# Kernel optimization log

Hardware: AMD Instinct MI355X
Metric: run time of the kernel (lower is better)

Reference implementation:

```python
import jax, jax.numpy as jnp
import numpy as np

EMB = 256
HID = 256
NH = 8
HD = HID // NH  # 32
EPS = 1e-5


def _wn(v, g):
    # torch weight_norm(dim=0): per-output-row normalization of v
    return g[:, None] * v / jnp.linalg.norm(v, axis=1, keepdims=True)


def _ln(x, gamma, beta):
    mu = jnp.mean(x, axis=-1, keepdims=True)
    var = jnp.mean((x - mu) ** 2, axis=-1, keepdims=True)
    return (x - mu) * jax.lax.rsqrt(var + EPS) * gamma + beta


def _rope(x):
    # x: [B', S, H, D]; torchtune-style rotary embedding, base 10000
    S, D = x.shape[1], x.shape[3]
    freqs = 1.0 / (10000.0 ** (jnp.arange(0, D, 2, dtype=jnp.float32) / D))  # [D/2]
    ang = jnp.arange(S, dtype=jnp.float32)[:, None] * freqs[None, :]          # [S, D/2]
    cos = jnp.cos(ang)[None, :, None, :]
    sin = jnp.sin(ang)[None, :, None, :]
    xr = x.reshape(*x.shape[:-1], D // 2, 2)
    x0, x1 = xr[..., 0], xr[..., 1]
    out = jnp.stack([x0 * cos - x1 * sin, x1 * cos + x0 * sin], axis=-1)
    return out.reshape(x.shape)


def setup_inputs() -> dict:
    key = jax.random.key(0)
    ks = jax.random.split(key, 12)
    s = lambda shp: 0.02
    return {
        "z": jax.random.normal(ks[0], (2, 32, 512, EMB), dtype=jnp.float32),
        "ln1_g": jnp.ones((EMB,), jnp.float32),
        "ln1_b": jnp.zeros((EMB,), jnp.float32),
        "proj_v": jax.random.normal(ks[1], (3 * HID, EMB), jnp.float32) * 0.02,
        "proj_g": jnp.ones((3 * HID,), jnp.float32),
        "proj_b": jnp.zeros((3 * HID,), jnp.float32),
        "ff_v": jax.random.normal(ks[2], (EMB, HID), jnp.float32) * 0.02,
        "ff_g": jnp.ones((EMB,), jnp.float32),
        "ff_b": jnp.zeros((EMB,), jnp.float32),
        "ln2_g": jnp.ones((EMB,), jnp.float32),
        "ln2_b": jnp.zeros((EMB,), jnp.float32),
        "w1_v": jax.random.normal(ks[3], (EMB, EMB), jnp.float32) * 0.02,
        "w1_g": jnp.ones((EMB,), jnp.float32),
        "w1_b": jnp.zeros((EMB,), jnp.float32),
        "w2_v": jax.random.normal(ks[4], (EMB, EMB), jnp.float32) * 0.02,
        "w2_g": jnp.ones((EMB,), jnp.float32),
        "w2_b": jnp.zeros((EMB,), jnp.float32),
    }


def reference(z, ln1_g, ln1_b, proj_v, proj_g, proj_b, ff_v, ff_g, ff_b,
              ln2_g, ln2_b, w1_v, w1_g, w1_b, w2_v, w2_g, w2_b):
    B, U, A, E = z.shape
    BU = B * U
    Wqkv = _wn(proj_v, proj_g)   # [3H, E]
    Wo = _wn(ff_v, ff_g)         # [E, H]
    # ---- RoPE attention block ----
    z_ = _ln(z, ln1_g, ln1_b).reshape(BU, A, E)
    qkv = z_ @ Wqkv.T + proj_b                       # [BU, A, 3H]
    qkv = qkv.reshape(BU, A, NH, 3 * HD)
    q, k, v = jnp.split(qkv, 3, axis=-1)             # each [BU, A, NH, HD]
    q = _rope(q)
    k = _rope(k)
    qh = q.transpose(0, 2, 1, 3)                     # [BU, NH, A, HD]
    kh = k.transpose(0, 2, 1, 3)
    vh = v.transpose(0, 2, 1, 3)
    scores = jnp.einsum('bhqd,bhkd->bhqk', qh, kh) / jnp.sqrt(jnp.float32(HD))
    attn = jax.nn.softmax(scores, axis=-1)
    out = jnp.einsum('bhqk,bhkd->bhqd', attn, vh)    # [BU, NH, A, HD]
    out = out.transpose(0, 2, 1, 3).reshape(BU, A, HID)
    out = out @ Wo.T + ff_b
    z = z + out.reshape(B, U, A, E)
    # ---- NormFF block ----
    W1 = _wn(w1_v, w1_g)
    W2 = _wn(w2_v, w2_g)
    h = _ln(z, ln2_g, ln2_b)
    h = jax.nn.gelu(h @ W1.T + w1_b, approximate=False)
    h = h @ W2.T + w2_b
    return z + h
```

## Files before the change

kernel.cpp:

```cpp
#include <hip/hip_runtime.h>
#include <cmath>

#define EMB 256
#define NHEAD 8
#define HD 32
#define A_LEN 512
#define TOK 32768

typedef __bf16 bf16_t;
typedef __bf16 bf16x8 __attribute__((ext_vector_type(8)));
typedef __bf16 bf16x4 __attribute__((ext_vector_type(4)));
typedef float floatx4 __attribute__((ext_vector_type(4)));

#define MFMA16(a, b, c) __builtin_amdgcn_mfma_f32_16x16x32_bf16((a), (b), (c), 0, 0, 0)

__global__ __launch_bounds__(64) void setup_kernel(
    const float* __restrict__ proj_v, const float* __restrict__ proj_g,
    const float* __restrict__ ff_v, const float* __restrict__ ff_g,
    const float* __restrict__ w1_v, const float* __restrict__ w1_g,
    const float* __restrict__ w2_v, const float* __restrict__ w2_g,
    bf16_t* __restrict__ Wall, float* __restrict__ ctab,
    float* __restrict__ stab) {
    int b = blockIdx.x;
    int lane = threadIdx.x;
    if (b < 1536) {
        const float* v; const float* g; int r;
        if (b < 768)       { v = proj_v; g = proj_g; r = b; }
        else if (b < 1024) { v = ff_v;   g = ff_g;   r = b - 768; }
        else if (b < 1280) { v = w1_v;   g = w1_g;   r = b - 1024; }
        else               { v = w2_v;   g = w2_g;   r = b - 1280; }
        const floatx4* vr = (const floatx4*)(v + (size_t)r * 256);
        floatx4 x = vr[lane];
        float ss = x[0] * x[0] + x[1] * x[1] + x[2] * x[2] + x[3] * x[3];
#pragma unroll
        for (int off = 32; off >= 1; off >>= 1) ss += __shfl_xor(ss, off);
        float sc = g[r] * rsqrtf(ss);
        bf16x4 o;
        o[0] = (bf16_t)(x[0] * sc); o[1] = (bf16_t)(x[1] * sc);
        o[2] = (bf16_t)(x[2] * sc); o[3] = (bf16_t)(x[3] * sc);
        ((bf16x4*)(Wall + (size_t)b * 256))[lane] = o;
    } else {
        int idx = (b - 1536) * 64 + lane;
        int a = idx >> 4, i = idx & 15;
        float freq = expf(-(float)(2 * i) * 0.2878231366242558f);
        float ang = (float)a * freq;
        ctab[idx] = cosf(ang);
        stab[idx] = sinf(ang);
    }
}

__global__ __launch_bounds__(256, 4) void qkv_kernel(
    const float* __restrict__ z, const float* __restrict__ ln_g,
    const float* __restrict__ ln_b, const bf16_t* __restrict__ W,
    const float* __restrict__ pb, const float* __restrict__ ctab,
    const float* __restrict__ stab, bf16_t* __restrict__ qbf,
    bf16_t* __restrict__ kbf, bf16_t* __restrict__ vtb) {
    __shared__ bf16_t xns[32 * 264];
    __shared__ bf16_t vls[256 * 40];
    int tid = threadIdx.x;
    int t0 = blockIdx.x * 32;

#pragma unroll
    for (int it = 0; it < 2; ++it) {
        int row = it * 16 + (tid >> 4);
        int sub = tid & 15;
        const floatx4* zr = (const floatx4*)(z + (size_t)(t0 + row) * 256 + sub * 16);
        floatx4 v0 = zr[0], v1 = zr[1], v2 = zr[2], v3 = zr[3];
        float vals[16];
        ((floatx4*)vals)[0] = v0; ((floatx4*)vals)[1] = v1;
        ((floatx4*)vals)[2] = v2; ((floatx4*)vals)[3] = v3;
        float s = 0.f, q2 = 0.f;
#pragma unroll
        for (int i = 0; i < 16; ++i) { s += vals[i]; q2 += vals[i] * vals[i]; }
#pragma unroll
        for (int off = 8; off >= 1; off >>= 1) {
            s += __shfl_xor(s, off);
            q2 += __shfl_xor(q2, off);
        }
        float mu = s * (1.f / 256.f);
        float inv = rsqrtf(q2 * (1.f / 256.f) - mu * mu + 1e-5f);
        int cb = sub * 16;
        bf16x8 o0, o1;
#pragma unroll
        for (int i = 0; i < 8; ++i)
            o0[i] = (bf16_t)((vals[i] - mu) * inv * ln_g[cb + i] + ln_b[cb + i]);
#pragma unroll
        for (int i = 0; i < 8; ++i)
            o1[i] = (bf16_t)((vals[8 + i] - mu) * inv * ln_g[cb + 8 + i] + ln_b[cb + 8 + i]);
        *(bf16x8*)&xns[row * 264 + cb] = o0;
        *(bf16x8*)&xns[row * 264 + cb + 8] = o1;
    }
    __syncthreads();

    int wv = tid >> 6, lane = tid & 63, quad = lane >> 4, lidx = lane & 15;

#pragma unroll 1
    for (int g = 0; g < 3; ++g) {
        floatx4 acc[4][2];
#pragma unroll
        for (int i = 0; i < 4; ++i) {
            acc[i][0] = (floatx4){0.f, 0.f, 0.f, 0.f};
            acc[i][1] = (floatx4){0.f, 0.f, 0.f, 0.f};
        }
#pragma unroll 2
        for (int kc = 0; kc < 8; ++kc) {
            bf16x8 a0 = *(const bf16x8*)&xns[lidx * 264 + kc * 32 + quad * 8];
            bf16x8 a1 = *(const bf16x8*)&xns[(16 + lidx) * 264 + kc * 32 + quad * 8];
#pragma unroll
            for (int ntl = 0; ntl < 4; ++ntl) {
                int n = wv * 192 + (g * 4 + ntl) * 16 + lidx;
                bf16x8 bfr = *(const bf16x8*)&W[(size_t)n * 256 + kc * 32 + quad * 8];
                acc[ntl][0] = MFMA16(a0, bfr, acc[ntl][0]);
                acc[ntl][1] = MFMA16(a1, bfr, acc[ntl][1]);
            }
        }
#pragma unroll
        for (int ntl = 0; ntl < 4; ++ntl) {
            int nbase = wv * 192 + (g * 4 + ntl) * 16;
            int n = nbase + lidx;
            float bias = pb[n];
            int htile = nbase / 96;
            int rem = nbase % 96;
            int sec = rem >> 5;
            int d = (rem & 31) + lidx;
#pragma unroll
            for (int mt = 0; mt < 2; ++mt) {
#pragma unroll
                for (int r = 0; r < 4; ++r) {
                    int a_loc = mt * 16 + quad * 4 + r;
                    int tok = t0 + a_loc;
                    int a = tok & 511;
                    int bu = tok >> 9;
                    float val = acc[ntl][mt][r] + bias;
                    if (sec == 2) {
                        vls[(htile * 32 + d) * 40 + a_loc] = (bf16_t)val;
                    } else {
                        size_t addr = ((size_t)((bu * 8 + htile) * 512 + a)) * 32 + d;
                        float part = __shfl_xor(val, 1);
                        float cs = ctab[a * 16 + (d >> 1)];
                        float sn = stab[a * 16 + (d >> 1)];
                        float res = ((d & 1) == 0) ? (val * cs - part * sn)
                                                   : (val * cs + part * sn);
                        if (sec == 0)
                            qbf[addr] = (bf16_t)(res * 0.17677669529663687f);
                        else
                            kbf[addr] = (bf16_t)res;
                    }
                }
            }
        }
    }
    __syncthreads();
    {
        int bu = t0 >> 9, ac0 = t0 & 511;
        size_t gbase = ((size_t)(bu * 256 + tid)) * 512 + ac0;
#pragma unroll
        for (int j = 0; j < 4; ++j)
            *(bf16x8*)&vtb[gbase + j * 8] = *(const bf16x8*)&vls[tid * 40 + j * 8];
    }
}

__global__ __launch_bounds__(512, 4) void attn_kernel(
    const bf16_t* __restrict__ qbf, const bf16_t* __restrict__ kbf,
    const bf16_t* __restrict__ vtb, bf16_t* __restrict__ ob) {
    __shared__ bf16_t Kls[512 * 32];
    __shared__ bf16_t Vt[32 * 512];
    __shared__ bf16_t Pls[8 * 16 * 64];
    int tid = threadIdx.x;
    int wv = tid >> 6, lane = tid & 63, quad = lane >> 4, lidx = lane & 15;
    int bh = blockIdx.x;
    int bu = bh >> 3, h = bh & 7;
    size_t hb = (size_t)bh * (A_LEN * HD);

#pragma unroll
    for (int i = 0; i < 4; ++i) {
        int c = tid + i * 512;
        int key = c >> 2, blk = c & 3;
        bf16x8 kv = *(const bf16x8*)&kbf[hb + (size_t)c * 8];
        *(bf16x8*)&Kls[key * 32 + ((blk ^ (key & 3)) << 3)] = kv;
        int vrow = c >> 6, vblk = c & 63;
        bf16x8 vv = *(const bf16x8*)&vtb[hb + (size_t)c * 8];
        *(bf16x8*)&Vt[vrow * 512 + ((vblk ^ (vrow & 7)) << 3)] = vv;
    }
    __syncthreads();

    int pbase = wv * (16 * 64);
    const floatx4 cm8 = (floatx4){-8.f, -8.f, -8.f, -8.f};
    const floatx4 zero4 = (floatx4){0.f, 0.f, 0.f, 0.f};

#pragma unroll 1
    for (int mt = 0; mt < 4; ++mt) {
        int q0 = wv * 64 + mt * 16;
        bf16x8 qfrag = *(const bf16x8*)&qbf[hb + (size_t)(q0 + lidx) * 32 + quad * 8];
        float l_[4] = {0.f, 0.f, 0.f, 0.f};
        floatx4 Oacc[2];
        Oacc[0] = zero4; Oacc[1] = zero4;

#pragma unroll 1
        for (int kc = 0; kc < 8; ++kc) {
            floatx4 sc[4];
#pragma unroll
            for (int t = 0; t < 4; ++t) {
                bf16x8 kf = *(const bf16x8*)&Kls[(kc * 64 + t * 16 + lidx) * 32 +
                                                 ((quad ^ (lidx & 3)) << 3)];
                sc[t] = MFMA16(qfrag, kf, cm8);
            }
            float p[4][4];
#pragma unroll
            for (int t = 0; t < 4; ++t)
#pragma unroll
                for (int r = 0; r < 4; ++r) p[t][r] = __expf(sc[t][r]);
#pragma unroll
            for (int t = 0; t < 4; ++t)
#pragma unroll
                for (int r = 0; r < 4; ++r) {
                    int row = quad * 4 + r;
                    int pc = (t * 16 + lidx) ^ ((row & 7) << 3);
                    Pls[pbase + row * 64 + pc] = (bf16_t)p[t][r];
                }
#pragma unroll
            for (int r = 0; r < 4; ++r) {
                float s = (p[0][r] + p[1][r]) + (p[2][r] + p[3][r]);
#pragma unroll
                for (int off = 8; off >= 1; off >>= 1) s += __shfl_xor(s, off);
                l_[r] += s;
            }
#pragma unroll
            for (int ks = 0; ks < 2; ++ks) {
                bf16x8 pf = *(const bf16x8*)&Pls[pbase + lidx * 64 +
                                                 (((ks * 4 + quad) ^ (lidx & 7)) << 3)];
#pragma unroll
                for (int nt = 0; nt < 2; ++nt) {
                    int vrow = nt * 16 + lidx;
                    bf16x8 vf = *(const bf16x8*)&Vt[vrow * 512 +
                        ((kc * 8 + ((ks * 4 + quad) ^ (lidx & 7))) << 3)];
                    Oacc[nt] = MFMA16(pf, vf, Oacc[nt]);
                }
            }
        }
#pragma unroll
        for (int nt = 0; nt < 2; ++nt)
#pragma unroll
            for (int r = 0; r < 4; ++r) {
                int tok = bu * 512 + q0 + quad * 4 + r;
                ob[(size_t)tok * 256 + h * 32 + nt * 16 + lidx] =
                    (bf16_t)(Oacc[nt][r] / l_[r]);
            }
    }
}

__global__ __launch_bounds__(256, 4) void tail_kernel(
    const bf16_t* __restrict__ X, const bf16_t* __restrict__ Wo,
    const float* __restrict__ obias, const float* __restrict__ zin,
    const float* __restrict__ ln_g, const float* __restrict__ ln_b,
    const bf16_t* __restrict__ W1, const float* __restrict__ b1,
    const bf16_t* __restrict__ W2, const float* __restrict__ b2,
    float* __restrict__ outp) {
    __shared__ float fbuf[32 * 264];
    __shared__ float red[32 * 8];
    __shared__ float mi[32 * 2];
    bf16_t* xbuf = (bf16_t*)fbuf;
    int tid = threadIdx.x;
    int t0 = blockIdx.x * 32;
    int wv = tid >> 6, lane = tid & 63, quad = lane >> 4, lidx = lane & 15;

    {
        int row = tid >> 3;
        int c0 = (tid & 7) * 32;
        const bf16x8* src = (const bf16x8*)&X[(size_t)(t0 + row) * 256 + c0];
        bf16x8* dst = (bf16x8*)&xbuf[row * 264 + c0];
        dst[0] = src[0]; dst[1] = src[1]; dst[2] = src[2]; dst[3] = src[3];
    }
    __syncthreads();

    float r1[4][2][4];
    {
        floatx4 acc[4][2];
#pragma unroll
        for (int i = 0; i < 4; ++i) {
            acc[i][0] = (floatx4){0.f, 0.f, 0.f, 0.f};
            acc[i][1] = (floatx4){0.f, 0.f, 0.f, 0.f};
        }
#pragma unroll 2
        for (int kc = 0; kc < 8; ++kc) {
            bf16x8 a0 = *(const bf16x8*)&xbuf[lidx * 264 + kc * 32 + quad * 8];
            bf16x8 a1 = *(const bf16x8*)&xbuf[(16 + lidx) * 264 + kc * 32 + quad * 8];
#pragma unroll
            for (int nt = 0; nt < 4; ++nt) {
                int n = wv * 64 + nt * 16 + lidx;
                bf16x8 bfr = *(const bf16x8*)&Wo[(size_t)n * 256 + kc * 32 + quad * 8];
                acc[nt][0] = MFMA16(a0, bfr, acc[nt][0]);
                acc[nt][1] = MFMA16(a1, bfr, acc[nt][1]);
            }
        }
#pragma unroll
        for (int nt = 0; nt < 4; ++nt) {
            int n = wv * 64 + nt * 16 + lidx;
            float b = obias[n];
#pragma unroll
            for (int mt = 0; mt < 2; ++mt)
#pragma unroll
                for (int r = 0; r < 4; ++r) {
                    size_t o = (size_t)(t0 + mt * 16 + quad * 4 + r) * 256 + n;
                    r1[nt][mt][r] = zin[o] + acc[nt][mt][r] + b;
                }
        }
    }

#pragma unroll
    for (int mt = 0; mt < 2; ++mt)
#pragma unroll
        for (int r = 0; r < 4; ++r) {
            float s = 0.f, ss = 0.f;
#pragma unroll
            for (int nt = 0; nt < 4; ++nt) {
                float v = r1[nt][mt][r];
                s += v; ss += v * v;
            }
#pragma unroll
            for (int off = 8; off >= 1; off >>= 1) {
                s += __shfl_xor(s, off);
                ss += __shfl_xor(ss, off);
            }
            if (lidx == 0) {
                int row = mt * 16 + quad * 4 + r;
                red[row * 8 + wv * 2] = s;
                red[row * 8 + wv * 2 + 1] = ss;
            }
        }
    __syncthreads();
    if (tid < 32) {
        float s = 0.f, ss = 0.f;
#pragma unroll
        for (int w = 0; w < 4; ++w) {
            s += red[tid * 8 + w * 2];
            ss += red[tid * 8 + w * 2 + 1];
        }
        float mu = s * (1.f / 256.f);
        mi[tid * 2] = mu;
        mi[tid * 2 + 1] = rsqrtf(ss * (1.f / 256.f) - mu * mu + 1e-5f);
    }
    __syncthreads();

    {
        float gv[4], bv[4];
#pragma unroll
        for (int nt = 0; nt < 4; ++nt) {
            int n = wv * 64 + nt * 16 + lidx;
            gv[nt] = ln_g[n]; bv[nt] = ln_b[n];
        }
#pragma unroll
        for (int mt = 0; mt < 2; ++mt)
#pragma unroll
            for (int r = 0; r < 4; ++r) {
                int row = mt * 16 + quad * 4 + r;
                float mu = mi[row * 2], inv = mi[row * 2 + 1];
#pragma unroll
                for (int nt = 0; nt < 4; ++nt) {
                    int n = wv * 64 + nt * 16 + lidx;
                    xbuf[row * 264 + n] =
                        (bf16_t)((r1[nt][mt][r] - mu) * inv * gv[nt] + bv[nt]);
                }
            }
    }
    __syncthreads();

    {
        floatx4 acc[4][2];
#pragma unroll
        for (int i = 0; i < 4; ++i) {
            acc[i][0] = (floatx4){0.f, 0.f, 0.f, 0.f};
            acc[i][1] = (floatx4){0.f, 0.f, 0.f, 0.f};
        }
#pragma unroll 2
        for (int kc = 0; kc < 8; ++kc) {
            bf16x8 a0 = *(const bf16x8*)&xbuf[lidx * 264 + kc * 32 + quad * 8];
            bf16x8 a1 = *(const bf16x8*)&xbuf[(16 + lidx) * 264 + kc * 32 + quad * 8];
#pragma unroll
            for (int nt = 0; nt < 4; ++nt) {
                int n = wv * 64 + nt * 16 + lidx;
                bf16x8 bfr = *(const bf16x8*)&W1[(size_t)n * 256 + kc * 32 + quad * 8];
                acc[nt][0] = MFMA16(a0, bfr, acc[nt][0]);
                acc[nt][1] = MFMA16(a1, bfr, acc[nt][1]);
            }
        }
        __syncthreads();
#pragma unroll
        for (int nt = 0; nt < 4; ++nt) {
            int n = wv * 64 + nt * 16 + lidx;
            float b = b1[n];
#pragma unroll
            for (int mt = 0; mt < 2; ++mt)
#pragma unroll
                for (int r = 0; r < 4; ++r) {
                    float x = acc[nt][mt][r] + b;
                    float gel = 0.5f * x * (1.f + erff(x * 0.7071067811865476f));
                    xbuf[(mt * 16 + quad * 4 + r) * 264 + n] = (bf16_t)gel;
                }
        }
    }
    __syncthreads();

    {
        floatx4 acc[4][2];
#pragma unroll
        for (int i = 0; i < 4; ++i) {
            acc[i][0] = (floatx4){0.f, 0.f, 0.f, 0.f};
            acc[i][1] = (floatx4){0.f, 0.f, 0.f, 0.f};
        }
#pragma unroll 2
        for (int kc = 0; kc < 8; ++kc) {
            bf16x8 a0 = *(const bf16x8*)&xbuf[lidx * 264 + kc * 32 + quad * 8];
            bf16x8 a1 = *(const bf16x8*)&xbuf[(16 + lidx) * 264 + kc * 32 + quad * 8];
#pragma unroll
            for (int nt = 0; nt < 4; ++nt) {
                int n = wv * 64 + nt * 16 + lidx;
                bf16x8 bfr = *(const bf16x8*)&W2[(size_t)n * 256 + kc * 32 + quad * 8];
                acc[nt][0] = MFMA16(a0, bfr, acc[nt][0]);
                acc[nt][1] = MFMA16(a1, bfr, acc[nt][1]);
            }
        }
        __syncthreads();
#pragma unroll
        for (int nt = 0; nt < 4; ++nt) {
            int n = wv * 64 + nt * 16 + lidx;
            float b = b2[n];
#pragma unroll
            for (int mt = 0; mt < 2; ++mt)
#pragma unroll
                for (int r = 0; r < 4; ++r)
                    fbuf[(mt * 16 + quad * 4 + r) * 264 + n] =
                        r1[nt][mt][r] + acc[nt][mt][r] + b;
        }
    }
    __syncthreads();

#pragma unroll
    for (int i = 0; i < 8; ++i) {
        int fid = i * 256 + tid;
        int row = fid >> 6;
        int c4 = (fid & 63) * 4;
        *(floatx4*)&outp[(size_t)(t0 + row) * 256 + c4] =
            *(const floatx4*)&fbuf[row * 264 + c4];
    }
}

extern "C" void kernel_launch(void* const* d_in, const int* in_sizes, int n_in,
                              void* d_out, int out_size, void* d_ws, size_t ws_size,
                              hipStream_t stream) {
    const float* z      = (const float*)d_in[0];
    const float* ln1_g  = (const float*)d_in[1];
    const float* ln1_b  = (const float*)d_in[2];
    const float* proj_v = (const float*)d_in[3];
    const float* proj_g = (const float*)d_in[4];
    const float* proj_b = (const float*)d_in[5];
    const float* ff_v   = (const float*)d_in[6];
    const float* ff_g   = (const float*)d_in[7];
    const float* ff_b   = (const float*)d_in[8];
    const float* ln2_g  = (const float*)d_in[9];
    const float* ln2_b  = (const float*)d_in[10];
    const float* w1_v   = (const float*)d_in[11];
    const float* w1_g   = (const float*)d_in[12];
    const float* w1_b   = (const float*)d_in[13];
    const float* w2_v   = (const float*)d_in[14];
    const float* w2_g   = (const float*)d_in[15];
    const float* w2_b   = (const float*)d_in[16];
    float* out = (float*)d_out;

    char* p = (char*)d_ws;
    bf16_t* Wall = (bf16_t*)p; p += (size_t)1536 * 256 * 2;
    float* ctab  = (float*)p;  p += 8192 * 4;
    float* stab  = (float*)p;  p += 8192 * 4;
    bf16_t* qbf  = (bf16_t*)p; p += (size_t)TOK * 256 * 2;
    bf16_t* kbf  = (bf16_t*)p; p += (size_t)TOK * 256 * 2;
    bf16_t* vtb  = (bf16_t*)p; p += (size_t)TOK * 256 * 2;
    bf16_t* abuf = (bf16_t*)p; p += (size_t)TOK * 256 * 2;

    const bf16_t* Wqkv = Wall;
    const bf16_t* Wo   = Wall + (size_t)768 * 256;
    const bf16_t* W1   = Wall + (size_t)1024 * 256;
    const bf16_t* W2   = Wall + (size_t)1280 * 256;

    setup_kernel<<<1664, 64, 0, stream>>>(proj_v, proj_g, ff_v, ff_g,
                                          w1_v, w1_g, w2_v, w2_g,
                                          Wall, ctab, stab);
    qkv_kernel<<<TOK / 32, 256, 0, stream>>>(z, ln1_g, ln1_b, Wqkv, proj_b,
                                             ctab, stab, qbf, kbf, vtb);
    attn_kernel<<<64 * 8, 512, 0, stream>>>(qbf, kbf, vtb, abuf);
    tail_kernel<<<TOK / 32, 256, 0, stream>>>(abuf, Wo, ff_b, z, ln2_g, ln2_b,
                                              W1, w1_b, W2, w2_b, out);
}
```

Measured before the change: 294.6 us.

## Restructure QKV epilogue for in-register RoPE and coalesced LDS-staged stores

The QKV projection is now split into separate Q, K and V passes. For Q and K the MFMA operands are swapped so each lane holds four consecutive head-dim values, which lets RoPE run in registers without cross-lane shuffles. The bias is preloaded into the accumulators, and results are staged through shared memory so global writes become 16-byte coalesced chunks instead of scattered 2-byte stores. This adds extra barriers and a larger staging buffer, and the V staging uses a 34-element stride that does not keep 128-bit LDS reads 16-byte aligned.

```diff
diff --git a/kernel.cpp b/kernel.cpp
--- a/kernel.cpp
+++ b/kernel.cpp
@@ -56,9 +56,10 @@
     const float* __restrict__ stab, bf16_t* __restrict__ qbf,
     bf16_t* __restrict__ kbf, bf16_t* __restrict__ vtb) {
     __shared__ bf16_t xns[32 * 264];
-    __shared__ bf16_t vls[256 * 40];
+    __shared__ bf16_t stg[8704];
     int tid = threadIdx.x;
     int t0 = blockIdx.x * 32;
+    int bu = t0 >> 9, a0 = t0 & 511;
 
 #pragma unroll
     for (int it = 0; it < 2; ++it) {
@@ -95,68 +96,103 @@
     int wv = tid >> 6, lane = tid & 63, quad = lane >> 4, lidx = lane & 15;
 
 #pragma unroll 1
-    for (int g = 0; g < 3; ++g) {
+    for (int sec = 0; sec < 2; ++sec) {
+        bf16_t* __restrict__ dst = (sec == 0) ? qbf : kbf;
         floatx4 acc[4][2];
 #pragma unroll
-        for (int i = 0; i < 4; ++i) {
-            acc[i][0] = (floatx4){0.f, 0.f, 0.f, 0.f};
-            acc[i][1] = (floatx4){0.f, 0.f, 0.f, 0.f};
+        for (int ntl = 0; ntl < 4; ++ntl) {
+            int cb = wv * 64 + ntl * 16;
+            int ht = cb >> 5;
+            floatx4 b4 = *(const floatx4*)&pb[ht * 96 + sec * 32 + (cb & 31) + quad * 4];
+            acc[ntl][0] = b4; acc[ntl][1] = b4;
         }
 #pragma unroll 2
         for (int kc = 0; kc < 8; ++kc) {
-            bf16x8 a0 = *(const bf16x8*)&xns[lidx * 264 + kc * 32 + quad * 8];
-            bf16x8 a1 = *(const bf16x8*)&xns[(16 + lidx) * 264 + kc * 32 + quad * 8];
+            bf16x8 x0 = *(const bf16x8*)&xns[lidx * 264 + kc * 32 + quad * 8];
+            bf16x8 x1 = *(const bf16x8*)&xns[(16 + lidx) * 264 + kc * 32 + quad * 8];
 #pragma unroll
             for (int ntl = 0; ntl < 4; ++ntl) {
-                int n = wv * 192 + (g * 4 + ntl) * 16 + lidx;
-                bf16x8 bfr = *(const bf16x8*)&W[(size_t)n * 256 + kc * 32 + quad * 8];
-                acc[ntl][0] = MFMA16(a0, bfr, acc[ntl][0]);
-                acc[ntl][1] = MFMA16(a1, bfr, acc[ntl][1]);
-            }
-        }
+                int cb = wv * 64 + ntl * 16;
+                int ht = cb >> 5;
+                int n = ht * 96 + sec * 32 + (cb & 31) + lidx;
+                bf16x8 wf = *(const bf16x8*)&W[(size_t)n * 256 + kc * 32 + quad * 8];
+                acc[ntl][0] = MFMA16(wf, x0, acc[ntl][0]);
+                acc[ntl][1] = MFMA16(wf, x1, acc[ntl][1]);
+            }
+        }
+        float scl = (sec == 0) ? 0.17677669529663687f : 1.0f;
 #pragma unroll
         for (int ntl = 0; ntl < 4; ++ntl) {
-            int nbase = wv * 192 + (g * 4 + ntl) * 16;
-            int n = nbase + lidx;
-            float bias = pb[n];
-            int htile = nbase / 96;
-            int rem = nbase % 96;
-            int sec = rem >> 5;
-            int d = (rem & 31) + lidx;
-#pragma unroll
-            for (int mt = 0; mt < 2; ++mt) {
-#pragma unroll
-                for (int r = 0; r < 4; ++r) {
-                    int a_loc = mt * 16 + quad * 4 + r;
-                    int tok = t0 + a_loc;
-                    int a = tok & 511;
-                    int bu = tok >> 9;
-                    float val = acc[ntl][mt][r] + bias;
-                    if (sec == 2) {
-                        vls[(htile * 32 + d) * 40 + a_loc] = (bf16_t)val;
-                    } else {
-                        size_t addr = ((size_t)((bu * 8 + htile) * 512 + a)) * 32 + d;
-                        float part = __shfl_xor(val, 1);
-                        float cs = ctab[a * 16 + (d >> 1)];
-                        float sn = stab[a * 16 + (d >> 1)];
-                        float res = ((d & 1) == 0) ? (val * cs - part * sn)
-                                                   : (val * cs + part * sn);
-                        if (sec == 0)
-                            qbf[addr] = (bf16_t)(res * 0.17677669529663687f);
-                        else
-                            kbf[addr] = (bf16_t)res;
-                    }
-                }
-            }
-        }
-    }
-    __syncthreads();
+            int cb = wv * 64 + ntl * 16;
+            int d0 = (cb & 31) + quad * 4;
+            int fi = d0 >> 1;
+#pragma unroll
+            for (int tt = 0; tt < 2; ++tt) {
+                int al = tt * 16 + lidx;
+                int a = a0 + al;
+                float cs0 = ctab[a * 16 + fi],     cs1 = ctab[a * 16 + fi + 1];
+                float sn0 = stab[a * 16 + fi],     sn1 = stab[a * 16 + fi + 1];
+                floatx4 v = acc[ntl][tt];
+                bf16x4 o;
+                o[0] = (bf16_t)((v[0] * cs0 - v[1] * sn0) * scl);
+                o[1] = (bf16_t)((v[1] * cs0 + v[0] * sn0) * scl);
+                o[2] = (bf16_t)((v[2] * cs1 - v[3] * sn1) * scl);
+                o[3] = (bf16_t)((v[3] * cs1 + v[2] * sn1) * scl);
+                *(bf16x4*)&stg[al * 264 + cb + quad * 4] = o;
+            }
+        }
+        __syncthreads();
+#pragma unroll
+        for (int i = 0; i < 4; ++i) {
+            int cid = i * 256 + tid;
+            int chunk = cid & 3, al = (cid >> 2) & 31, ht = cid >> 7;
+            bf16x8 vv = *(const bf16x8*)&stg[al * 264 + ht * 32 + chunk * 8];
+            *(bf16x8*)&dst[((size_t)((bu * 8 + ht) * 512 + a0 + al)) * 32 + chunk * 8] = vv;
+        }
+        __syncthreads();
+    }
+
     {
-        int bu = t0 >> 9, ac0 = t0 & 511;
-        size_t gbase = ((size_t)(bu * 256 + tid)) * 512 + ac0;
-#pragma unroll
-        for (int j = 0; j < 4; ++j)
-            *(bf16x8*)&vtb[gbase + j * 8] = *(const bf16x8*)&vls[tid * 40 + j * 8];
+        floatx4 acc[4][2];
+#pragma unroll
+        for (int ntl = 0; ntl < 4; ++ntl) {
+            int cb = wv * 64 + ntl * 16;
+            int ht = cb >> 5;
+            float b = pb[ht * 96 + 64 + (cb & 31) + lidx];
+            acc[ntl][0] = (floatx4){b, b, b, b};
+            acc[ntl][1] = (floatx4){b, b, b, b};
+        }
+#pragma unroll 2
+        for (int kc = 0; kc < 8; ++kc) {
+            bf16x8 x0 = *(const bf16x8*)&xns[lidx * 264 + kc * 32 + quad * 8];
+            bf16x8 x1 = *(const bf16x8*)&xns[(16 + lidx) * 264 + kc * 32 + quad * 8];
+#pragma unroll
+            for (int ntl = 0; ntl < 4; ++ntl) {
+                int cb = wv * 64 + ntl * 16;
+                int ht = cb >> 5;
+                int n = ht * 96 + 64 + (cb & 31) + lidx;
+                bf16x8 wf = *(const bf16x8*)&W[(size_t)n * 256 + kc * 32 + quad * 8];
+                acc[ntl][0] = MFMA16(x0, wf, acc[ntl][0]);
+                acc[ntl][1] = MFMA16(x1, wf, acc[ntl][1]);
+            }
+        }
+#pragma unroll
+        for (int ntl = 0; ntl < 4; ++ntl) {
+            int vcol = wv * 64 + ntl * 16 + lidx;
+#pragma unroll
+            for (int tt = 0; tt < 2; ++tt)
+#pragma unroll
+                for (int r = 0; r < 4; ++r)
+                    stg[vcol * 34 + tt * 16 + quad * 4 + r] = (bf16_t)acc[ntl][tt][r];
+        }
+        __syncthreads();
+#pragma unroll
+        for (int i = 0; i < 4; ++i) {
+            int cid = i * 256 + tid;
+            int chunk = cid & 3, vcol = cid >> 2;
+            bf16x8 vv = *(const bf16x8*)&stg[vcol * 34 + chunk * 8];
+            *(bf16x8*)&vtb[((size_t)(bu * 256 + vcol)) * 512 + a0 + chunk * 8] = vv;
+        }
     }
 }
 
```

After: 279.0 us. 5.3% less time.
